# Kernel optimization log

Hardware: AMD Instinct MI355X
Metric: run time of the kernel (lower is better)

## Reference

```python
import jax, jax.numpy as jnp
import numpy as np

LMAX = 4
NCOEF = (LMAX + 1) ** 2  # 25 spherical-harmonic coefficients
EXPAND = np.repeat(np.arange(LMAX + 1), [2 * l + 1 for l in range(LMAX + 1)])  # per-l -> per-(l,m)
N, E, C, H, HEADS, ACH, VCH, F, G, DE, AEMB, MAXEL = 10000, 50000, 64, 64, 8, 16, 8, 128, 36, 32, 32, 100


def setup_inputs() -> dict:
    ks = jax.random.split(jax.random.key(0), 24)
    f = lambda i, shape, s=1.0: jax.random.normal(ks[i], shape, jnp.float32) * s
    return dict(
        x=f(0, (N, NCOEF, C)),
        edge_index=jax.random.randint(ks[1], (2, E), 0, N),
        atomic_numbers=jax.random.randint(ks[2], (N,), 0, MAXEL),
        edge_distance=jax.random.uniform(ks[3], (E, DE), jnp.float32),
        wigner=f(4, (E, NCOEF, NCOEF), 0.2),
        src_tab=f(5, (MAXEL, AEMB), 0.02), tgt_tab=f(6, (MAXEL, AEMB), 0.02),
        rad_w1=f(7, (DE + 2 * AEMB, 64), 0.1), rad_b1=jnp.zeros((64,), jnp.float32),
        rad_w2=f(8, (64, 64), 0.1), rad_b2=jnp.zeros((64,), jnp.float32),
        rad_w3=f(9, (64, (LMAX + 1) * 2 * C), 0.05), rad_b3=jnp.ones(((LMAX + 1) * 2 * C,), jnp.float32),
        W1=f(10, (2 * C, H), 0.05), W0_extra=f(11, (2 * C, HEADS * ACH + H), 0.05),
        alpha_dot=f(12, (HEADS, ACH), 0.1),
        to_grid=f(13, (G, NCOEF), 0.2), from_grid=f(14, (NCOEF, G), 0.2),
        proj_out=f(15, (HEADS * VCH, C), 0.1),
        gamma1=jnp.ones((C,), jnp.float32), gamma2=jnp.ones((C,), jnp.float32),
        gl_w=f(16, (C, F), 0.1), gl_b=jnp.zeros((F,), jnp.float32),
        ffn_w1=f(17, (C, F), 0.1), ffn_b1=jnp.zeros((F,), jnp.float32),
        ffn_w2=f(18, (F, C), 0.1), ffn_b2=jnp.zeros((C,), jnp.float32),
    )


def _rmsnorm(x, gamma, eps=1e-6):
    # equivariant norm over the coefficient axis, per node/channel
    rms = jnp.sqrt(jnp.mean(x * x, axis=1, keepdims=True) + eps)  # [N,1,C]
    return x / rms * gamma


def _s2_sep_act(gate, x, to_grid, from_grid):
    # separable S2 activation: scalars = silu(gating scalars); l>0 via grid SiLU
    grid = jnp.einsum('gi,nih->ngh', to_grid, x)
    xg = jnp.einsum('ig,ngh->nih', from_grid, jax.nn.silu(grid))
    return jnp.concatenate([jax.nn.silu(gate)[:, None, :], xg[:, 1:, :]], axis=1)


def reference(x, edge_index, atomic_numbers, edge_distance, wigner, src_tab, tgt_tab,
              rad_w1, rad_b1, rad_w2, rad_b2, rad_w3, rad_b3,
              W1, W0_extra, alpha_dot, to_grid, from_grid, proj_out,
              gamma1, gamma2, gl_w, gl_b, ffn_w1, ffn_b1, ffn_w2, ffn_b2):
    src, dst = edge_index[0], edge_index[1]
    # ---- SO2 equivariant graph attention (gather -> rotate -> conv -> act -> attn -> scatter) ----
    h = _rmsnorm(x, gamma1)
    xe = jnp.concatenate([h[src], h[dst]], axis=-1)          # [E,25,2C] edge gather
    xe = jnp.einsum('eij,ejc->eic', wigner, xe)              # rotate into edge frame
    ef = jnp.concatenate([edge_distance, src_tab[atomic_numbers[src]],
                          tgt_tab[atomic_numbers[dst]]], axis=-1)
    r = jax.nn.silu(ef @ rad_w1 + rad_b1)
    r = jax.nn.silu(r @ rad_w2 + rad_b2)
    r = (r @ rad_w3 + rad_b3).reshape(-1, LMAX + 1, 2 * C)[:, EXPAND, :]  # m-shared radial, [E,25,2C]
    xe = xe * r
    extra = xe[:, 0, :] @ W0_extra                           # extra m=0 channels
    alpha_f = extra[:, :HEADS * ACH].reshape(-1, HEADS, ACH)
    gate = extra[:, HEADS * ACH:]                            # [E,H]
    msg = jnp.einsum('eic,ch->eih', xe, W1)                  # [E,25,H]
    msg = _s2_sep_act(gate, msg, to_grid, from_grid)
    # attention weights: softmax over incoming edges of each destination node
    alpha = jnp.einsum('eha,ha->eh', jax.nn.silu(alpha_f), alpha_dot)
    amax = jax.lax.stop_gradient(jax.ops.segment_max(alpha, dst, num_segments=N))
    a = jnp.exp(alpha - amax[dst])
    a = a / (jax.ops.segment_sum(a, dst, num_segments=N)[dst] + 1e-8)
    msg = (msg.reshape(-1, NCOEF, HEADS, VCH) * a[:, None, :, None]).reshape(-1, NCOEF, HEADS * VCH)
    msg = jnp.einsum('eji,ejc->eic', wigner, msg)            # rotate back (D^T)
    agg = jax.ops.segment_sum(msg, dst, num_segments=N)      # scatter-add, [N,25,H]
    x = x + agg @ proj_out
    # ---- feed-forward with separable S2 activation ----
    h = _rmsnorm(x, gamma2)
    gate = h[:, 0, :] @ gl_w + gl_b
    f1 = jnp.einsum('nic,cf->nif', h, ffn_w1)
    f1 = jnp.concatenate([f1[:, :1, :] + ffn_b1, f1[:, 1:, :]], axis=1)  # bias on l=0 only
    f1 = _s2_sep_act(gate, f1, to_grid, from_grid)
    f2 = jnp.einsum('nif,fc->nic', f1, ffn_w2)
    f2 = jnp.concatenate([f2[:, :1, :] + ffn_b2, f2[:, 1:, :]], axis=1)
    return x + f2
```

## Files before the change

kernel.cpp:

```cpp
#include <hip/hip_runtime.h>
#include <hip/hip_bf16.h>

#define NN 10000
#define NE 50000

typedef __attribute__((ext_vector_type(8))) short bfrag8;
typedef __attribute__((ext_vector_type(4))) short s16x4;
typedef __attribute__((ext_vector_type(4))) float f32x4;

__device__ __forceinline__ float silu_f(float v){ return v / (1.0f + __expf(-v)); }
__device__ __forceinline__ short f2b(float f){
  unsigned u = __float_as_uint(f);
  u += 0x7fffu + ((u>>16)&1u);
  return (short)(u>>16);
}
__device__ __forceinline__ float b2f(short s){
  return __uint_as_float(((unsigned)(unsigned short)s)<<16);
}

__global__ __launch_bounds__(256) void k_rms1(const float* __restrict__ x,
                                              const float* __restrict__ gamma,
                                              __hip_bfloat16* __restrict__ h){
  int idx = blockIdx.x*256 + threadIdx.x;
  if (idx >= NN*64) return;
  int n = idx>>6, c = idx&63;
  const float* xp = x + (size_t)n*1600 + c;
  float ss = 0.f;
#pragma unroll
  for (int i=0;i<25;i++){ float v = xp[i*64]; ss += v*v; }
  float inv = gamma[c] * rsqrtf(ss*(1.f/25.f) + 1e-6f);
  __hip_bfloat16* hp = h + (size_t)n*1600 + c;
#pragma unroll
  for (int i=0;i<25;i++) hp[i*64] = __float2bfloat16(xp[i*64]*inv);
}

__global__ void k_wprep(const float* __restrict__ W1, const float* __restrict__ tog,
                        const float* __restrict__ fromg, const float* __restrict__ proj,
                        const float* __restrict__ fw1, const float* __restrict__ fw2,
                        const float* __restrict__ rw1, const float* __restrict__ rw2,
                        const float* __restrict__ rw3, const float* __restrict__ w0e,
                        short* __restrict__ w1t, short* __restrict__ togA,
                        short* __restrict__ fgA, short* __restrict__ projT,
                        short* __restrict__ fw1T, short* __restrict__ fw2T,
                        short* __restrict__ rw1T, short* __restrict__ rw2T,
                        short* __restrict__ rw3T, short* __restrict__ w0eP){
  int t0 = blockIdx.x*blockDim.x + threadIdx.x;
  int stride = gridDim.x*blockDim.x;
  for (int idx=t0; idx<64*136; idx+=stride){
    int hh = idx/136, k = idx-136*hh;
    w1t[idx] = (k<128) ? f2b(W1[k*64+hh]) : (short)0;
  }
  for (int idx=t0; idx<48*40; idx+=stride){
    int g = idx/40, i = idx-40*g;
    togA[idx] = (g<36 && i<25) ? f2b(tog[g*25+i]) : (short)0;
  }
  for (int idx=t0; idx<32*72; idx+=stride){
    int j = idx/72, g = idx-72*j;
    fgA[idx] = (j<25 && g<36) ? f2b(fromg[j*36+g]) : (short)0;
  }
  for (int idx=t0; idx<64*64; idx+=stride){
    int c = idx>>6, k = idx&63;
    projT[idx] = f2b(proj[k*64+c]);
  }
  for (int idx=t0; idx<128*64; idx+=stride){
    int f = idx>>6, c = idx&63;
    fw1T[idx] = f2b(fw1[c*128+f]);
  }
  for (int idx=t0; idx<64*128; idx+=stride){
    int c = idx>>7, f = idx&127;
    fw2T[idx] = f2b(fw2[f*64+c]);
  }
  for (int idx=t0; idx<64*96; idx+=stride){
    int n = idx/96, k = idx-96*n;
    rw1T[idx] = f2b(rw1[k*64+n]);
  }
  for (int idx=t0; idx<64*64; idx+=stride){
    int n = idx>>6, k = idx&63;
    rw2T[idx] = f2b(rw2[k*64+n]);
  }
  for (int idx=t0; idx<640*64; idx+=stride){
    int n = idx>>6, k = idx&63;
    rw3T[idx] = f2b(rw3[(size_t)k*640+n]);
  }
  for (int idx=t0; idx<128*192; idx+=stride)
    w0eP[idx] = f2b(w0e[idx]);
}

__global__ __launch_bounds__(256,4) void k_radial(
  const int* __restrict__ ei, const int* __restrict__ an,
  const float* __restrict__ edist,
  const float* __restrict__ stab, const float* __restrict__ ttab,
  const short* __restrict__ rw1T, const float* __restrict__ rb1,
  const short* __restrict__ rw2T, const float* __restrict__ rb2,
  const short* __restrict__ rw3T, const float* __restrict__ rb3,
  short* __restrict__ rfS)
{
  __shared__ __align__(16) short SP[7936];
  const int tid = threadIdx.x;
  const int wv = tid>>6, lane = tid&63, lo = lane&15, q = lane>>4;
  const int e0 = blockIdx.x*32;
  {
    int e = tid>>3;
    int ee = min(e0+e, NE-1);
    int srcE = ei[ee], dstE = ei[NE+ee];
    const float* dp = edist + (size_t)ee*32;
    const float* sp = stab + (size_t)an[srcE]*32;
    const float* tp = ttab + (size_t)an[dstE]*32;
    int kb = tid&7;
#pragma unroll
    for (int it=0; it<12; ++it){
      int k = kb + it*8;
      float v = (k<32) ? dp[k] : (k<64 ? sp[k-32] : tp[k-64]);
      SP[e*104+k] = f2b(v);
    }
  }
  __syncthreads();
  {
    f32x4 zf={0.f,0.f,0.f,0.f}; f32x4 acc[2]={zf,zf};
#pragma unroll
    for (int kt=0;kt<3;kt++){
      bfrag8 a = *(const bfrag8*)&rw1T[(wv*16+lo)*96 + kt*32 + q*8];
#pragma unroll
      for (int et=0;et<2;et++){
        bfrag8 b = *(const bfrag8*)&SP[(et*16+lo)*104 + kt*32 + q*8];
        acc[et] = __builtin_amdgcn_mfma_f32_16x16x32_bf16(a,b,acc[et],0,0,0);
      }
    }
    int n1 = wv*16 + q*4;
    const float4 bb = *(const float4*)&rb1[n1];
#pragma unroll
    for (int et=0;et<2;et++){
      s16x4 o;
      o[0]=f2b(silu_f(acc[et][0]+bb.x)); o[1]=f2b(silu_f(acc[et][1]+bb.y));
      o[2]=f2b(silu_f(acc[et][2]+bb.z)); o[3]=f2b(silu_f(acc[et][3]+bb.w));
      *(s16x4*)&SP[3328 + (et*16+lo)*72 + n1] = o;
    }
  }
  __syncthreads();
  {
    f32x4 zf={0.f,0.f,0.f,0.f}; f32x4 acc[2]={zf,zf};
#pragma unroll
    for (int kt=0;kt<2;kt++){
      bfrag8 a = *(const bfrag8*)&rw2T[(wv*16+lo)*64 + kt*32 + q*8];
#pragma unroll
      for (int et=0;et<2;et++){
        bfrag8 b = *(const bfrag8*)&SP[3328 + (et*16+lo)*72 + kt*32 + q*8];
        acc[et] = __builtin_amdgcn_mfma_f32_16x16x32_bf16(a,b,acc[et],0,0,0);
      }
    }
    int n2 = wv*16 + q*4;
    const float4 bb = *(const float4*)&rb2[n2];
#pragma unroll
    for (int et=0;et<2;et++){
      s16x4 o;
      o[0]=f2b(silu_f(acc[et][0]+bb.x)); o[1]=f2b(silu_f(acc[et][1]+bb.y));
      o[2]=f2b(silu_f(acc[et][2]+bb.z)); o[3]=f2b(silu_f(acc[et][3]+bb.w));
      *(s16x4*)&SP[5632 + (et*16+lo)*72 + n2] = o;
    }
  }
  __syncthreads();
  {
    bfrag8 bfr[2][2];
#pragma unroll
    for (int et=0;et<2;et++)
#pragma unroll
      for (int kt=0;kt<2;kt++)
        bfr[et][kt] = *(const bfrag8*)&SP[5632 + (et*16+lo)*72 + kt*32 + q*8];
    for (int mi=0; mi<10; ++mi){
      int n3base = (wv + mi*4)*16;
      f32x4 zf={0.f,0.f,0.f,0.f}; f32x4 acc[2]={zf,zf};
#pragma unroll
      for (int kt=0;kt<2;kt++){
        bfrag8 a = *(const bfrag8*)&rw3T[(size_t)(n3base+lo)*64 + kt*32 + q*8];
        acc[0] = __builtin_amdgcn_mfma_f32_16x16x32_bf16(a,bfr[0][kt],acc[0],0,0,0);
        acc[1] = __builtin_amdgcn_mfma_f32_16x16x32_bf16(a,bfr[1][kt],acc[1],0,0,0);
      }
      int n3 = n3base + q*4;
      const float4 bb = *(const float4*)&rb3[n3];
#pragma unroll
      for (int et=0;et<2;et++){
        int e = e0 + et*16 + lo;
        if (e < NE){
          s16x4 o;
          o[0]=f2b(acc[et][0]+bb.x); o[1]=f2b(acc[et][1]+bb.y);
          o[2]=f2b(acc[et][2]+bb.z); o[3]=f2b(acc[et][3]+bb.w);
          *(s16x4*)&rfS[(size_t)e*640 + n3] = o;
        }
      }
    }
  }
}

__global__ __launch_bounds__(256,4) void k_edge(
  const __hip_bfloat16* __restrict__ h, const int* __restrict__ ei,
  const float* __restrict__ wig,
  const short* __restrict__ w1t, const short* __restrict__ togA,
  const short* __restrict__ fgA, const short* __restrict__ w0eP,
  const float* __restrict__ adot,
  const short* __restrict__ rfS, float* __restrict__ asum,
  float* __restrict__ agg)
{
  __shared__ __align__(16) short POOL[16288];
  float* rfull = (float*)&POOL[14592];
  float* gateL = (float*)&POOL[15872];
  float* ahead = (float*)&POOL[16000];
  float* exL   = (float*)&POOL[16032];
  const int tid = threadIdx.x;
  const int wv = tid>>6, lane = tid&63, lo = lane&15, q = lane>>4;
  const int e = blockIdx.x;
  const int src = ei[e], dst = ei[NE+e];

  {
    int4 z; z.x=0; z.y=0; z.z=0; z.w=0;
    int4* zp = (int4*)POOL;
    for (int idx=tid; idx<960; idx+=256) zp[idx] = z;
  }
  __syncthreads();
  for (int idx=tid; idx<625; idx+=256){
    int i = idx/25, j = idx-25*i;
    short v = f2b(wig[(size_t)e*625+idx]);
    POOL[5120 + i*40 + j] = v;
    POOL[6400 + j*40 + i] = v;
  }
  {
    const __hip_bfloat16* hs = h + (size_t)src*1600;
    const __hip_bfloat16* hd = h + (size_t)dst*1600;
    for (int idx=tid; idx<400; idx+=256){
      int nh = idx/200, rem = idx-200*nh;
      int j = rem>>3, cg = rem&7;
      const __hip_bfloat16* hp = nh ? hd : hs;
      uint4 v = *(const uint4*)(hp + j*64 + cg*8);
      unsigned el[8] = {v.x&0xffffu, v.x>>16, v.y&0xffffu, v.y>>16,
                        v.z&0xffffu, v.z>>16, v.w&0xffffu, v.w>>16};
      int cb = nh*64 + cg*8;
#pragma unroll
      for (int qq=0;qq<8;qq++) POOL[(cb+qq)*40 + j] = (short)el[qq];
    }
  }
  for (int idx=tid; idx<640; idx+=256) rfull[idx] = b2f(rfS[(size_t)e*640+idx]);
  __syncthreads();

  {
    f32x4 zf = {0.f,0.f,0.f,0.f};
    f32x4 acc[2][2] = {{zf,zf},{zf,zf}};
    bfrag8 b0 = *(const bfrag8*)&POOL[5120 + (lo)*40 + q*8];
    bfrag8 b1 = *(const bfrag8*)&POOL[5120 + (16+lo)*40 + q*8];
#pragma unroll
    for (int t=0;t<2;t++){
      int mrow = (2*wv+t)*16 + lo;
      bfrag8 a = *(const bfrag8*)&POOL[mrow*40 + q*8];
      acc[t][0] = __builtin_amdgcn_mfma_f32_16x16x32_bf16(a, b0, acc[t][0], 0,0,0);
      acc[t][1] = __builtin_amdgcn_mfma_f32_16x16x32_bf16(a, b1, acc[t][1], 0,0,0);
    }
#pragma unroll
    for (int t=0;t<2;t++){
      int c0 = (2*wv+t)*16 + q*4;
#pragma unroll
      for (int nt=0;nt<2;nt++){
        int i = nt*16 + lo;
        int l = (i>=16)?4:((i>=9)?3:((i>=4)?2:((i>=1)?1:0)));
        const f32x4 rv = *(const f32x4*)&rfull[l*128 + c0];
        s16x4 o;
#pragma unroll
        for (int r=0;r<4;r++) o[r] = f2b(acc[t][nt][r]*rv[r]);
        *(s16x4*)&POOL[7680 + i*136 + c0] = o;
      }
    }
  }
  __syncthreads();

  {
    if (tid < 96){
      float s0=0.f, s1=0.f;
      for (int c=0; c<128; c+=2){
        unsigned xp = *(const unsigned*)&POOL[7680 + c];
        float x0 = b2f((short)(xp&0xffffu)), x1 = b2f((short)(xp>>16));
        unsigned wp0 = *(const unsigned*)&w0eP[c*192 + 2*tid];
        unsigned wp1 = *(const unsigned*)&w0eP[(c+1)*192 + 2*tid];
        s0 += x0*b2f((short)(wp0&0xffffu)) + x1*b2f((short)(wp1&0xffffu));
        s1 += x0*b2f((short)(wp0>>16))     + x1*b2f((short)(wp1>>16));
      }
      if (tid < 64){
        int n0 = 2*tid;
        exL[n0]   = silu_f(s0)*adot[n0];
        exL[n0+1] = silu_f(s1)*adot[n0+1];
      } else {
        int g0 = 2*tid - 128;
        gateL[g0]   = silu_f(s0);
        gateL[g0+1] = silu_f(s1);
      }
    }
  }
  {
    const int hh = wv*16 + lo;
    f32x4 zf = {0.f,0.f,0.f,0.f};
    f32x4 acc[2] = {zf,zf};
#pragma unroll
    for (int kt=0;kt<4;kt++){
      bfrag8 b = *(const bfrag8*)&w1t[hh*136 + kt*32 + q*8];
#pragma unroll
      for (int t=0;t<2;t++){
        bfrag8 a = *(const bfrag8*)&POOL[7680 + (t*16+lo)*136 + kt*32 + q*8];
        acc[t] = __builtin_amdgcn_mfma_f32_16x16x32_bf16(a, b, acc[t], 0,0,0);
      }
    }
#pragma unroll
    for (int t=0;t<2;t++){
      s16x4 o;
#pragma unroll
      for (int r=0;r<4;r++) o[r] = f2b(acc[t][r]);
      *(s16x4*)&POOL[12032 + hh*40 + t*16 + q*4] = o;
    }
  }
  __syncthreads();

  if (tid < 8){
    float s = 0.f;
#pragma unroll
    for (int a=0;a<16;a++) s += exL[tid*16+a];
    float eh = __expf(s);
    ahead[tid] = eh;
    unsafeAtomicAdd(&asum[(size_t)dst*8 + tid], eh);
  }
  {
    const int hh = wv*16 + lo;
    bfrag8 b = *(const bfrag8*)&POOL[12032 + hh*40 + q*8];
    f32x4 zf = {0.f,0.f,0.f,0.f};
    f32x4 acc[3] = {zf,zf,zf};
#pragma unroll
    for (int t=0;t<3;t++){
      bfrag8 a = *(const bfrag8*)&togA[(t*16+lo)*40 + q*8];
      acc[t] = __builtin_amdgcn_mfma_f32_16x16x32_bf16(a, b, acc[t], 0,0,0);
    }
#pragma unroll
    for (int t=0;t<3;t++){
      s16x4 o;
#pragma unroll
      for (int r=0;r<4;r++) o[r] = f2b(silu_f(acc[t][r]));
      *(s16x4*)&POOL[hh*72 + t*16 + q*4] = o;
    }
  }
  __syncthreads();

  {
    const int hh = wv*16 + lo;
    f32x4 zf = {0.f,0.f,0.f,0.f};
    f32x4 acc[2] = {zf,zf};
#pragma unroll
    for (int kt=0;kt<2;kt++){
      bfrag8 b = *(const bfrag8*)&POOL[hh*72 + kt*32 + q*8];
#pragma unroll
      for (int t=0;t<2;t++){
        bfrag8 a = *(const bfrag8*)&fgA[(t*16+lo)*72 + kt*32 + q*8];
        acc[t] = __builtin_amdgcn_mfma_f32_16x16x32_bf16(a, b, acc[t], 0,0,0);
      }
    }
    float ah = ahead[hh>>3];
#pragma unroll
    for (int t=0;t<2;t++){
      s16x4 o;
#pragma unroll
      for (int r=0;r<4;r++){
        int j = t*16 + q*4 + r;
        float v = acc[t][r];
        if (j==0) v = gateL[hh];
        o[r] = f2b(v*ah);
      }
      *(s16x4*)&POOL[7680 + hh*40 + t*16 + q*4] = o;
    }
  }
  __syncthreads();

  {
    const int hh = wv*16 + lo;
    bfrag8 b = *(const bfrag8*)&POOL[7680 + hh*40 + q*8];
    f32x4 zf = {0.f,0.f,0.f,0.f};
    f32x4 acc[2] = {zf,zf};
#pragma unroll
    for (int t=0;t<2;t++){
      bfrag8 a = *(const bfrag8*)&POOL[6400 + (t*16+lo)*40 + q*8];
      acc[t] = __builtin_amdgcn_mfma_f32_16x16x32_bf16(a, b, acc[t], 0,0,0);
    }
    float* aggp = agg + (size_t)dst*1600;
#pragma unroll
    for (int t=0;t<2;t++){
#pragma unroll
      for (int r=0;r<4;r++){
        int i = t*16 + q*4 + r;
        if (i<25) unsafeAtomicAdd(&aggp[i*64+hh], acc[t][r]);
      }
    }
  }
}

__global__ __launch_bounds__(256,4) void k_node(
  const float* __restrict__ x, const float* __restrict__ aggin,
  const float* __restrict__ asum,
  const short* __restrict__ projT, const float* __restrict__ gamma2,
  const float* __restrict__ glw, const float* __restrict__ glb,
  const short* __restrict__ fw1T, const float* __restrict__ fb1,
  const short* __restrict__ fw2T, const float* __restrict__ fb2,
  const short* __restrict__ togA, const short* __restrict__ fgA,
  float* __restrict__ out)
{
  __shared__ __align__(16) short P[19072];
  float* xF    = (float*)P;
  short* sgB   = P + 4352;
  short* hh2B  = P + 4352;
  short* f1B   = P + 13568;
  short* aggB  = P + 13568;
  short* xgB   = P + 13568;
  float* invc  = ((float*)P) + 9344;
  float* gateF = ((float*)P) + 9408;
  const int tid = threadIdx.x;
  const int wv = tid>>6, lane = tid&63, lo = lane&15, q = lane>>4;
  const int n = blockIdx.x;
  const s16x4 z4 = {0,0,0,0};

  for (int idx=tid; idx<400; idx+=256){
    int i = idx>>4, k = idx&15;
    float sc = 1.f/(asum[(size_t)n*8 + (k>>1)] + 1e-8f);
    const float4 v = *(const float4*)(aggin + (size_t)n*1600 + (size_t)idx*4);
    s16x4 o; o[0]=f2b(v.x*sc); o[1]=f2b(v.y*sc); o[2]=f2b(v.z*sc); o[3]=f2b(v.w*sc);
    *(s16x4*)&aggB[i*72 + k*4] = o;
  }
  for (int idx=tid; idx<126; idx+=256)
    *(s16x4*)&hh2B[25*72 + idx*4] = z4;
  for (int idx=tid; idx<512; idx+=256){
    int f = idx>>2, gg = 48 + (idx&3)*4;
    *(s16x4*)&sgB[f*72 + gg] = z4;
  }
  __syncthreads();

  {
    f32x4 zf={0.f,0.f,0.f,0.f}; f32x4 acc[2]={zf,zf};
    const int c = wv*16 + lo;
#pragma unroll
    for (int kt=0;kt<2;kt++){
      bfrag8 b = *(const bfrag8*)&projT[c*64 + kt*32 + q*8];
#pragma unroll
      for (int t=0;t<2;t++){
        bfrag8 a = *(const bfrag8*)&aggB[(t*16+lo)*72 + kt*32 + q*8];
        acc[t] = __builtin_amdgcn_mfma_f32_16x16x32_bf16(a,b,acc[t],0,0,0);
      }
    }
#pragma unroll
    for (int t=0;t<2;t++)
#pragma unroll
      for (int r=0;r<4;r++){
        int i = t*16 + q*4 + r;
        if (i<25) xF[i*68+c] = acc[t][r] + x[(size_t)n*1600 + i*64 + c];
      }
  }
  __syncthreads();
  if (tid<64){
    float ss=0.f;
#pragma unroll
    for (int i=0;i<25;i++){ float v = xF[i*68+tid]; ss += v*v; }
    invc[tid] = gamma2[tid]*rsqrtf(ss*(1.f/25.f)+1e-6f);
  }
  __syncthreads();
  for (int idx=tid; idx<1600; idx+=256){
    int i=idx>>6, c=idx&63;
    hh2B[i*72+c] = f2b(xF[i*68+c]*invc[c]);
  }
  if (tid<128){
    float a = glb[tid];
#pragma unroll 8
    for (int c=0;c<64;c++) a += xF[c]*invc[c]*glw[c*128+tid];
    gateF[tid] = silu_f(a);
  }
  __syncthreads();

  {
    f32x4 zf={0.f,0.f,0.f,0.f}; f32x4 acc[2][2]={{zf,zf},{zf,zf}};
#pragma unroll
    for (int kt=0;kt<2;kt++){
      bfrag8 a0 = *(const bfrag8*)&hh2B[(lo)*72 + kt*32 + q*8];
      bfrag8 a1 = *(const bfrag8*)&hh2B[(16+lo)*72 + kt*32 + q*8];
#pragma unroll
      for (int s=0;s<2;s++){
        int f = wv*32 + s*16 + lo;
        bfrag8 b = *(const bfrag8*)&fw1T[f*64 + kt*32 + q*8];
        acc[0][s] = __builtin_amdgcn_mfma_f32_16x16x32_bf16(a0,b,acc[0][s],0,0,0);
        acc[1][s] = __builtin_amdgcn_mfma_f32_16x16x32_bf16(a1,b,acc[1][s],0,0,0);
      }
    }
#pragma unroll
    for (int s=0;s<2;s++){
      int f = wv*32 + s*16 + lo;
      float bb = fb1[f];
#pragma unroll
      for (int t=0;t<2;t++){
        s16x4 o;
#pragma unroll
        for (int r=0;r<4;r++){
          int i = t*16+q*4+r;
          o[r] = f2b(acc[t][s][r] + (i==0 ? bb : 0.f));
        }
        *(s16x4*)&f1B[f*40 + t*16 + q*4] = o;
      }
    }
  }
  __syncthreads();

  {
    f32x4 zf={0.f,0.f,0.f,0.f}; f32x4 acc[3][2]={{zf,zf},{zf,zf},{zf,zf}};
    bfrag8 a0 = *(const bfrag8*)&togA[(lo)*40 + q*8];
    bfrag8 a1 = *(const bfrag8*)&togA[(16+lo)*40 + q*8];
    bfrag8 a2 = *(const bfrag8*)&togA[(32+lo)*40 + q*8];
#pragma unroll
    for (int s=0;s<2;s++){
      int f = wv*32 + s*16 + lo;
      bfrag8 b = *(const bfrag8*)&f1B[f*40 + q*8];
      acc[0][s] = __builtin_amdgcn_mfma_f32_16x16x32_bf16(a0,b,acc[0][s],0,0,0);
      acc[1][s] = __builtin_amdgcn_mfma_f32_16x16x32_bf16(a1,b,acc[1][s],0,0,0);
      acc[2][s] = __builtin_amdgcn_mfma_f32_16x16x32_bf16(a2,b,acc[2][s],0,0,0);
    }
#pragma unroll
    for (int s=0;s<2;s++){
      int f = wv*32 + s*16 + lo;
#pragma unroll
      for (int t=0;t<3;t++){
        s16x4 o;
#pragma unroll
        for (int r=0;r<4;r++) o[r] = f2b(silu_f(acc[t][s][r]));
        *(s16x4*)&sgB[f*72 + t*16 + q*4] = o;
      }
    }
  }
  __syncthreads();

  {
    f32x4 zf={0.f,0.f,0.f,0.f}; f32x4 acc[2][2]={{zf,zf},{zf,zf}};
#pragma unroll
    for (int kt=0;kt<2;kt++){
#pragma unroll
      for (int t=0;t<2;t++){
        bfrag8 b = *(const bfrag8*)&fgA[(t*16+lo)*72 + kt*32 + q*8];
#pragma unroll
        for (int s=0;s<2;s++){
          bfrag8 a = *(const bfrag8*)&sgB[(wv*32+s*16+lo)*72 + kt*32 + q*8];
          acc[s][t] = __builtin_amdgcn_mfma_f32_16x16x32_bf16(a,b,acc[s][t],0,0,0);
        }
      }
    }
#pragma unroll
    for (int s=0;s<2;s++){
      int f0 = wv*32 + s*16 + q*4;
#pragma unroll
      for (int t=0;t<2;t++){
        int j = t*16 + lo;
        s16x4 o;
#pragma unroll
        for (int r=0;r<4;r++)
          o[r] = f2b(j==0 ? gateF[f0+r] : acc[s][t][r]);
        *(s16x4*)&xgB[j*136 + f0] = o;
      }
    }
  }
  __syncthreads();

  {
    f32x4 zf={0.f,0.f,0.f,0.f}; f32x4 acc[2]={zf,zf};
    const int c = wv*16 + lo;
#pragma unroll
    for (int kt=0;kt<4;kt++){
      bfrag8 b = *(const bfrag8*)&fw2T[c*128 + kt*32 + q*8];
#pragma unroll
      for (int t=0;t<2;t++){
        bfrag8 a = *(const bfrag8*)&xgB[(t*16+lo)*136 + kt*32 + q*8];
        acc[t] = __builtin_amdgcn_mfma_f32_16x16x32_bf16(a,b,acc[t],0,0,0);
      }
    }
    float bb = fb2[c];
#pragma unroll
    for (int t=0;t<2;t++)
#pragma unroll
      for (int r=0;r<4;r++){
        int i = t*16 + q*4 + r;
        if (i<25)
          out[(size_t)n*1600 + i*64 + c] = xF[i*68+c] + acc[t][r] + (i==0 ? bb : 0.f);
      }
  }
}

extern "C" void kernel_launch(void* const* d_in, const int* in_sizes, int n_in,
                              void* d_out, int out_size, void* d_ws, size_t ws_size,
                              hipStream_t stream) {
  (void)in_sizes; (void)n_in; (void)ws_size;
  const float* x     = (const float*)d_in[0];
  const int*   ei    = (const int*)d_in[1];
  const int*   an    = (const int*)d_in[2];
  const float* edist = (const float*)d_in[3];
  const float* wig   = (const float*)d_in[4];
  const float* stab  = (const float*)d_in[5];
  const float* ttab  = (const float*)d_in[6];
  const float* rw1   = (const float*)d_in[7];
  const float* rb1   = (const float*)d_in[8];
  const float* rw2   = (const float*)d_in[9];
  const float* rb2   = (const float*)d_in[10];
  const float* rw3   = (const float*)d_in[11];
  const float* rb3   = (const float*)d_in[12];
  const float* W1    = (const float*)d_in[13];
  const float* w0e   = (const float*)d_in[14];
  const float* adot  = (const float*)d_in[15];
  const float* tog   = (const float*)d_in[16];
  const float* fromg = (const float*)d_in[17];
  const float* proj  = (const float*)d_in[18];
  const float* g1    = (const float*)d_in[19];
  const float* g2    = (const float*)d_in[20];
  const float* glw   = (const float*)d_in[21];
  const float* glb   = (const float*)d_in[22];
  const float* fw1   = (const float*)d_in[23];
  const float* fb1   = (const float*)d_in[24];
  const float* fw2   = (const float*)d_in[25];
  const float* fb2   = (const float*)d_in[26];
  float* out = (float*)d_out;

  char* wsb = (char*)d_ws;
  __hip_bfloat16* hbuf = (__hip_bfloat16*)(wsb);
  short* rfS   = (short*)(wsb + 32000000);
  float* asum  = (float*)(wsb + 96000000);
  short* w1t   = (short*)(wsb + 96320128);
  short* togA  = (short*)(wsb + 96337600);
  short* fgA   = (short*)(wsb + 96341504);
  short* projT = (short*)(wsb + 96346112);
  short* fw1T  = (short*)(wsb + 96354304);
  short* fw2T  = (short*)(wsb + 96370688);
  short* rw1T  = (short*)(wsb + 96387072);
  short* rw2T  = (short*)(wsb + 96399360);
  short* rw3T  = (short*)(wsb + 96407552);
  short* w0eP  = (short*)(wsb + 96489472);

  hipMemsetAsync(asum, 0, (size_t)NN*8*sizeof(float), stream);
  hipMemsetAsync(d_out, 0, (size_t)out_size*sizeof(float), stream);

  k_wprep<<<32, 256, 0, stream>>>(W1, tog, fromg, proj, fw1, fw2, rw1, rw2, rw3, w0e,
                                  w1t, togA, fgA, projT, fw1T, fw2T,
                                  rw1T, rw2T, rw3T, w0eP);
  k_rms1  <<<(NN*64+255)/256, 256, 0, stream>>>(x, g1, hbuf);
  k_radial<<<(NE+31)/32, 256, 0, stream>>>(ei, an, edist, stab, ttab,
                                           rw1T, rb1, rw2T, rb2, rw3T, rb3, rfS);
  k_edge  <<<NE, 256, 0, stream>>>(hbuf, ei, wig, w1t, togA, fgA, w0eP, adot,
                                   rfS, asum, out);
  k_node  <<<NN, 256, 0, stream>>>(x, out, asum, projT, g2, glw, glb,
                                   fw1T, fb1, fw2T, fb2, togA, fgA, out);
}
```

Before: 1.115 ms.

## Store normalized features channel-major padded and feed MFMA directly from global

```diff
diff --git a/kernel.cpp b/kernel.cpp
--- a/kernel.cpp
+++ b/kernel.cpp
@@ -18,9 +18,9 @@
   return __uint_as_float(((unsigned)(unsigned short)s)<<16);
 }
 
-__global__ __launch_bounds__(256) void k_rms1(const float* __restrict__ x,
-                                              const float* __restrict__ gamma,
-                                              __hip_bfloat16* __restrict__ h){
+__global__ __launch_bounds__(256) void k_rms1T(const float* __restrict__ x,
+                                               const float* __restrict__ gamma,
+                                               short* __restrict__ hT){
   int idx = blockIdx.x*256 + threadIdx.x;
   if (idx >= NN*64) return;
   int n = idx>>6, c = idx&63;
@@ -29,9 +29,17 @@
 #pragma unroll
   for (int i=0;i<25;i++){ float v = xp[i*64]; ss += v*v; }
   float inv = gamma[c] * rsqrtf(ss*(1.f/25.f) + 1e-6f);
-  __hip_bfloat16* hp = h + (size_t)n*1600 + c;
-#pragma unroll
-  for (int i=0;i<25;i++) hp[i*64] = __float2bfloat16(xp[i*64]*inv);
+  short buf[32];
+#pragma unroll
+  for (int i=0;i<25;i++) buf[i] = f2b(xp[i*64]*inv);
+#pragma unroll
+  for (int i=25;i<32;i++) buf[i] = 0;
+  short* hp = hT + (size_t)n*2048 + c*32;
+#pragma unroll
+  for (int k=0;k<8;k++){
+    s16x4 o; o[0]=buf[k*4]; o[1]=buf[k*4+1]; o[2]=buf[k*4+2]; o[3]=buf[k*4+3];
+    *(s16x4*)&hp[k*4] = o;
+  }
 }
 
 __global__ void k_wprep(const float* __restrict__ W1, const float* __restrict__ tog,
@@ -43,7 +51,7 @@
                         short* __restrict__ fgA, short* __restrict__ projT,
                         short* __restrict__ fw1T, short* __restrict__ fw2T,
                         short* __restrict__ rw1T, short* __restrict__ rw2T,
-                        short* __restrict__ rw3T, short* __restrict__ w0eP){
+                        short* __restrict__ rw3T, float* __restrict__ w0eN){
   int t0 = blockIdx.x*blockDim.x + threadIdx.x;
   int stride = gridDim.x*blockDim.x;
   for (int idx=t0; idx<64*136; idx+=stride){
@@ -82,8 +90,10 @@
     int n = idx>>6, k = idx&63;
     rw3T[idx] = f2b(rw3[(size_t)k*640+n]);
   }
-  for (int idx=t0; idx<128*192; idx+=stride)
-    w0eP[idx] = f2b(w0e[idx]);
+  for (int idx=t0; idx<192*128; idx+=stride){
+    int n = idx>>7, c = idx&127;
+    w0eN[idx] = w0e[c*192+n];
+  }
 }
 
 __global__ __launch_bounds__(256,4) void k_radial(
@@ -192,50 +202,37 @@
 }
 
 __global__ __launch_bounds__(256,4) void k_edge(
-  const __hip_bfloat16* __restrict__ h, const int* __restrict__ ei,
+  const short* __restrict__ hT, const int* __restrict__ ei,
   const float* __restrict__ wig,
   const short* __restrict__ w1t, const short* __restrict__ togA,
-  const short* __restrict__ fgA, const short* __restrict__ w0eP,
+  const short* __restrict__ fgA, const float* __restrict__ w0eN,
   const float* __restrict__ adot,
   const short* __restrict__ rfS, float* __restrict__ asum,
   float* __restrict__ agg)
 {
-  __shared__ __align__(16) short POOL[16288];
-  float* rfull = (float*)&POOL[14592];
-  float* gateL = (float*)&POOL[15872];
-  float* ahead = (float*)&POOL[16000];
-  float* exL   = (float*)&POOL[16032];
+  __shared__ __align__(16) short POOL[16016];
+  float* rfull = (float*)&POOL[14080];
+  float* gateL = (float*)&POOL[15360];
+  float* ahead = (float*)&POOL[15488];
+  float* exL   = (float*)&POOL[15504];
+  float* xe0F  = (float*)&POOL[15760];
   const int tid = threadIdx.x;
   const int wv = tid>>6, lane = tid&63, lo = lane&15, q = lane>>4;
   const int e = blockIdx.x;
   const int src = ei[e], dst = ei[NE+e];
+  const short* hbase = hT + (size_t)(wv<2 ? src : dst)*2048;
 
   {
     int4 z; z.x=0; z.y=0; z.z=0; z.w=0;
     int4* zp = (int4*)POOL;
-    for (int idx=tid; idx<960; idx+=256) zp[idx] = z;
+    for (int idx=tid; idx<896; idx+=256) zp[idx] = z;
   }
   __syncthreads();
   for (int idx=tid; idx<625; idx+=256){
     int i = idx/25, j = idx-25*i;
     short v = f2b(wig[(size_t)e*625+idx]);
-    POOL[5120 + i*40 + j] = v;
-    POOL[6400 + j*40 + i] = v;
-  }
-  {
-    const __hip_bfloat16* hs = h + (size_t)src*1600;
-    const __hip_bfloat16* hd = h + (size_t)dst*1600;
-    for (int idx=tid; idx<400; idx+=256){
-      int nh = idx/200, rem = idx-200*nh;
-      int j = rem>>3, cg = rem&7;
-      const __hip_bfloat16* hp = nh ? hd : hs;
-      uint4 v = *(const uint4*)(hp + j*64 + cg*8);
-      unsigned el[8] = {v.x&0xffffu, v.x>>16, v.y&0xffffu, v.y>>16,
-                        v.z&0xffffu, v.z>>16, v.w&0xffffu, v.w>>16};
-      int cb = nh*64 + cg*8;
-#pragma unroll
-      for (int qq=0;qq<8;qq++) POOL[(cb+qq)*40 + j] = (short)el[qq];
-    }
+    POOL[4608 + i*40 + j] = v;
+    POOL[5888 + j*40 + i] = v;
   }
   for (int idx=tid; idx<640; idx+=256) rfull[idx] = b2f(rfS[(size_t)e*640+idx]);
   __syncthreads();
@@ -243,12 +240,12 @@
   {
     f32x4 zf = {0.f,0.f,0.f,0.f};
     f32x4 acc[2][2] = {{zf,zf},{zf,zf}};
-    bfrag8 b0 = *(const bfrag8*)&POOL[5120 + (lo)*40 + q*8];
-    bfrag8 b1 = *(const bfrag8*)&POOL[5120 + (16+lo)*40 + q*8];
+    bfrag8 b0 = *(const bfrag8*)&POOL[4608 + (lo)*40 + q*8];
+    bfrag8 b1 = *(const bfrag8*)&POOL[4608 + (16+lo)*40 + q*8];
 #pragma unroll
     for (int t=0;t<2;t++){
-      int mrow = (2*wv+t)*16 + lo;
-      bfrag8 a = *(const bfrag8*)&POOL[mrow*40 + q*8];
+      int crow = ((2*wv+t)*16 + lo) & 63;
+      bfrag8 a = *(const bfrag8*)&hbase[crow*32 + q*8];
       acc[t][0] = __builtin_amdgcn_mfma_f32_16x16x32_bf16(a, b0, acc[t][0], 0,0,0);
       acc[t][1] = __builtin_amdgcn_mfma_f32_16x16x32_bf16(a, b1, acc[t][1], 0,0,0);
     }
@@ -260,36 +257,33 @@
         int i = nt*16 + lo;
         int l = (i>=16)?4:((i>=9)?3:((i>=4)?2:((i>=1)?1:0)));
         const f32x4 rv = *(const f32x4*)&rfull[l*128 + c0];
+        f32x4 p;
+#pragma unroll
+        for (int r=0;r<4;r++) p[r] = acc[t][nt][r]*rv[r];
         s16x4 o;
 #pragma unroll
-        for (int r=0;r<4;r++) o[r] = f2b(acc[t][nt][r]*rv[r]);
-        *(s16x4*)&POOL[7680 + i*136 + c0] = o;
-      }
-    }
-  }
-  __syncthreads();
-
-  {
-    if (tid < 96){
-      float s0=0.f, s1=0.f;
-      for (int c=0; c<128; c+=2){
-        unsigned xp = *(const unsigned*)&POOL[7680 + c];
-        float x0 = b2f((short)(xp&0xffffu)), x1 = b2f((short)(xp>>16));
-        unsigned wp0 = *(const unsigned*)&w0eP[c*192 + 2*tid];
-        unsigned wp1 = *(const unsigned*)&w0eP[(c+1)*192 + 2*tid];
-        s0 += x0*b2f((short)(wp0&0xffffu)) + x1*b2f((short)(wp1&0xffffu));
-        s1 += x0*b2f((short)(wp0>>16))     + x1*b2f((short)(wp1>>16));
-      }
-      if (tid < 64){
-        int n0 = 2*tid;
-        exL[n0]   = silu_f(s0)*adot[n0];
-        exL[n0+1] = silu_f(s1)*adot[n0+1];
-      } else {
-        int g0 = 2*tid - 128;
-        gateL[g0]   = silu_f(s0);
-        gateL[g0+1] = silu_f(s1);
-      }
-    }
+        for (int r=0;r<4;r++) o[r] = f2b(p[r]);
+        *(s16x4*)&POOL[7168 + i*136 + c0] = o;
+        if (nt==0 && lo==0){
+          float4 pf; pf.x=p[0]; pf.y=p[1]; pf.z=p[2]; pf.w=p[3];
+          *(float4*)&xe0F[c0] = pf;
+        }
+      }
+    }
+  }
+  __syncthreads();
+
+  if (tid < 192){
+    float s = 0.f;
+    const float* wrow = w0eN + (size_t)tid*128;
+#pragma unroll 8
+    for (int kt=0; kt<32; ++kt){
+      const float4 xv = *(const float4*)&xe0F[kt*4];
+      const float4 wv4 = *(const float4*)&wrow[kt*4];
+      s += xv.x*wv4.x + xv.y*wv4.y + xv.z*wv4.z + xv.w*wv4.w;
+    }
+    if (tid < 128) exL[tid] = silu_f(s)*adot[tid];
+    else           gateL[tid-128] = silu_f(s);
   }
   {
     const int hh = wv*16 + lo;
@@ -300,7 +294,7 @@
       bfrag8 b = *(const bfrag8*)&w1t[hh*136 + kt*32 + q*8];
 #pragma unroll
       for (int t=0;t<2;t++){
-        bfrag8 a = *(const bfrag8*)&POOL[7680 + (t*16+lo)*136 + kt*32 + q*8];
+        bfrag8 a = *(const bfrag8*)&POOL[7168 + (t*16+lo)*136 + kt*32 + q*8];
         acc[t] = __builtin_amdgcn_mfma_f32_16x16x32_bf16(a, b, acc[t], 0,0,0);
       }
     }
@@ -309,7 +303,7 @@
       s16x4 o;
 #pragma unroll
       for (int r=0;r<4;r++) o[r] = f2b(acc[t][r]);
-      *(s16x4*)&POOL[12032 + hh*40 + t*16 + q*4] = o;
+      *(s16x4*)&POOL[11520 + hh*40 + t*16 + q*4] = o;
     }
   }
   __syncthreads();
@@ -324,7 +318,7 @@
   }
   {
     const int hh = wv*16 + lo;
-    bfrag8 b = *(const bfrag8*)&POOL[12032 + hh*40 + q*8];
+    bfrag8 b = *(const bfrag8*)&POOL[11520 + hh*40 + q*8];
     f32x4 zf = {0.f,0.f,0.f,0.f};
     f32x4 acc[3] = {zf,zf,zf};
 #pragma unroll
@@ -366,19 +360,19 @@
         if (j==0) v = gateL[hh];
         o[r] = f2b(v*ah);
       }
-      *(s16x4*)&POOL[7680 + hh*40 + t*16 + q*4] = o;
+      *(s16x4*)&POOL[7168 + hh*40 + t*16 + q*4] = o;
     }
   }
   __syncthreads();
 
   {
     const int hh = wv*16 + lo;
-    bfrag8 b = *(const bfrag8*)&POOL[7680 + hh*40 + q*8];
+    bfrag8 b = *(const bfrag8*)&POOL[7168 + hh*40 + q*8];
     f32x4 zf = {0.f,0.f,0.f,0.f};
     f32x4 acc[2] = {zf,zf};
 #pragma unroll
     for (int t=0;t<2;t++){
-      bfrag8 a = *(const bfrag8*)&POOL[6400 + (t*16+lo)*40 + q*8];
+      bfrag8 a = *(const bfrag8*)&POOL[5888 + (t*16+lo)*40 + q*8];
       acc[t] = __builtin_amdgcn_mfma_f32_16x16x32_bf16(a, b, acc[t], 0,0,0);
     }
     float* aggp = agg + (size_t)dst*1600;
@@ -619,30 +613,30 @@
   float* out = (float*)d_out;
 
   char* wsb = (char*)d_ws;
-  __hip_bfloat16* hbuf = (__hip_bfloat16*)(wsb);
-  short* rfS   = (short*)(wsb + 32000000);
-  float* asum  = (float*)(wsb + 96000000);
-  short* w1t   = (short*)(wsb + 96320128);
-  short* togA  = (short*)(wsb + 96337600);
-  short* fgA   = (short*)(wsb + 96341504);
-  short* projT = (short*)(wsb + 96346112);
-  short* fw1T  = (short*)(wsb + 96354304);
-  short* fw2T  = (short*)(wsb + 96370688);
-  short* rw1T  = (short*)(wsb + 96387072);
-  short* rw2T  = (short*)(wsb + 96399360);
-  short* rw3T  = (short*)(wsb + 96407552);
-  short* w0eP  = (short*)(wsb + 96489472);
+  short* hT    = (short*)(wsb);
+  short* rfS   = (short*)(wsb + 40960000);
+  float* asum  = (float*)(wsb + 104960000);
+  short* w1t   = (short*)(wsb + 105280000);
+  short* togA  = (short*)(wsb + 105297408);
+  short* fgA   = (short*)(wsb + 105301248);
+  short* projT = (short*)(wsb + 105305856);
+  short* fw1T  = (short*)(wsb + 105314048);
+  short* fw2T  = (short*)(wsb + 105330432);
+  short* rw1T  = (short*)(wsb + 105346816);
+  short* rw2T  = (short*)(wsb + 105359104);
+  short* rw3T  = (short*)(wsb + 105367296);
+  float* w0eN  = (float*)(wsb + 105449216);
 
   hipMemsetAsync(asum, 0, (size_t)NN*8*sizeof(float), stream);
   hipMemsetAsync(d_out, 0, (size_t)out_size*sizeof(float), stream);
 
   k_wprep<<<32, 256, 0, stream>>>(W1, tog, fromg, proj, fw1, fw2, rw1, rw2, rw3, w0e,
                                   w1t, togA, fgA, projT, fw1T, fw2T,
-                                  rw1T, rw2T, rw3T, w0eP);
-  k_rms1  <<<(NN*64+255)/256, 256, 0, stream>>>(x, g1, hbuf);
+                                  rw1T, rw2T, rw3T, w0eN);
+  k_rms1T <<<(NN*64+255)/256, 256, 0, stream>>>(x, g1, hT);
   k_radial<<<(NE+31)/32, 256, 0, stream>>>(ei, an, edist, stab, ttab,
                                            rw1T, rb1, rw2T, rb2, rw3T, rb3, rfS);
-  k_edge  <<<NE, 256, 0, stream>>>(hbuf, ei, wig, w1t, togA, fgA, w0eP, adot,
+  k_edge  <<<NE, 256, 0, stream>>>(hT, ei, wig, w1t, togA, fgA, w0eN, adot,
                                    rfS, asum, out);
   k_node  <<<NN, 256, 0, stream>>>(x, out, asum, projT, g2, glw, glb,
                                    fw1T, fb1, fw2T, fb2, togA, fgA, out);
```

After: 1.253 ms. 1.12x slower.
